# Optimization experiments

Measured on AMD Instinct MI355X. Metric: run time of the kernel, lower is better.

The kernel has to match this reference:

```python
import jax, jax.numpy as jnp
import numpy as np

B, S_IN, S_CTX = 2, 4096, 512
INPUT_DIM = CTX_DIM = DIM = 1024
NUM_HEADS = 16
HEAD_DIM = DIM // NUM_HEADS
BASE = 10000.0


def rms_norm(x, scale, eps=1e-6):
    xf = x.astype(jnp.float32)
    rrms = jax.lax.rsqrt(jnp.mean(xf * xf, axis=-1, keepdims=True) + eps)
    return (xf * rrms).astype(x.dtype) * scale


def apply_rope(x, pos):
    # x: [B, N, H, D]; rotate-half RoPE over full head_dim
    d = x.shape[-1]
    inv_freq = 1.0 / (BASE ** (jnp.arange(0, d, 2, dtype=jnp.float32) / d))  # [d/2]
    ang = pos.astype(jnp.float32)[:, None] * inv_freq[None, :]  # [N, d/2]
    cos = jnp.cos(ang)[None, :, None, :]
    sin = jnp.sin(ang)[None, :, None, :]
    x1, x2 = x[..., : d // 2], x[..., d // 2 :]
    return jnp.concatenate([x1 * cos - x2 * sin, x2 * cos + x1 * sin], axis=-1).astype(x.dtype)


def setup_inputs() -> dict:
    key = jax.random.key(0)
    ks = jax.random.split(key, 8)
    std = 0.02
    return {
        "input": jax.random.normal(ks[0], (B, S_IN, INPUT_DIM), jnp.float32),
        "context": jax.random.normal(ks[1], (B, S_CTX, CTX_DIM), jnp.float32),
        "W_qkv_in": jax.random.normal(ks[2], (3 * DIM, INPUT_DIM), jnp.float32) * std,
        "b_qkv_in": jnp.zeros((3 * DIM,), jnp.float32),
        "W_qkv_ctx": jax.random.normal(ks[3], (3 * DIM, CTX_DIM), jnp.float32) * std,
        "b_qkv_ctx": jnp.zeros((3 * DIM,), jnp.float32),
        "q_scale_in": jnp.ones((DIM,), jnp.float32),
        "k_scale_in": jnp.ones((DIM,), jnp.float32),
        "q_scale_ctx": jnp.ones((DIM,), jnp.float32),
        "k_scale_ctx": jnp.ones((DIM,), jnp.float32),
        "W_out_in": jax.random.normal(ks[4], (INPUT_DIM, DIM), jnp.float32) * std,
        "b_out_in": jnp.zeros((INPUT_DIM,), jnp.float32),
        "W_out_ctx": jax.random.normal(ks[5], (CTX_DIM, DIM), jnp.float32) * std,
        "b_out_ctx": jnp.zeros((CTX_DIM,), jnp.float32),
    }


def reference(input, context, W_qkv_in, b_qkv_in, W_qkv_ctx, b_qkv_ctx,
              q_scale_in, k_scale_in, q_scale_ctx, k_scale_ctx,
              W_out_in, b_out_in, W_out_ctx, b_out_ctx):
    # dual-stream QKV projections
    qkv_i = input @ W_qkv_in.T + b_qkv_in        # [B, S_in, 3*DIM]
    qkv_c = context @ W_qkv_ctx.T + b_qkv_ctx    # [B, S_ctx, 3*DIM]
    qi, ki, vi = jnp.split(qkv_i, 3, axis=-1)
    qc, kc, vc = jnp.split(qkv_c, 3, axis=-1)
    # QK-RMSNorm over full dim (as in QKNorm(dim))
    qi, ki = rms_norm(qi, q_scale_in), rms_norm(ki, k_scale_in)
    qc, kc = rms_norm(qc, q_scale_ctx), rms_norm(kc, k_scale_ctx)
    # concat context first, then input
    q = jnp.concatenate([qc, qi], axis=1)  # [B, N, DIM]
    k = jnp.concatenate([kc, ki], axis=1)
    v = jnp.concatenate([vc, vi], axis=1)
    N = q.shape[1]
    pos = jnp.arange(N)
    # RoPE applied per head
    q = apply_rope(q.reshape(B, N, NUM_HEADS, HEAD_DIM), pos).reshape(B, N, DIM)
    k = apply_rope(k.reshape(B, N, NUM_HEADS, HEAD_DIM), pos).reshape(B, N, DIM)
    # single-head attention over full dim (faithful to source: heads flattened before q@k^T)
    scale = HEAD_DIM ** -0.5
    attn = jax.nn.softmax(jnp.einsum('bnd,bmd->bnm', q, k) * scale, axis=-1)
    out = jnp.einsum('bnm,bmd->bnd', attn, v)  # [B, N, DIM]
    s_ctx = context.shape[1]
    input_output = out[:, s_ctx:, :] @ W_out_in.T + b_out_in
    context_output = out[:, :s_ctx, :] @ W_out_ctx.T + b_out_ctx
    return (input_output, context_output)
```

## Files before the change

### kernel.cpp

```cpp
#include <hip/hip_runtime.h>
#include <stdint.h>

typedef unsigned short u16;
typedef __bf16 bf16x8 __attribute__((ext_vector_type(8)));
typedef float f32x4 __attribute__((ext_vector_type(4)));

typedef const __attribute__((address_space(1))) uint32_t* gu32p;
typedef __attribute__((address_space(3))) uint32_t* lu32p;
#define GLOAD_LDS16(g, l) \
  __builtin_amdgcn_global_load_lds((gu32p)(const void*)(g), (lu32p)(void*)(l), 16, 0, 0)

static __device__ __forceinline__ u16 f2bf(float f) {
  uint32_t u = __builtin_bit_cast(uint32_t, f);
  return (u16)((u + 0x7FFFu + ((u >> 16) & 1u)) >> 16);
}
static __device__ __forceinline__ float bf2f(u16 h) {
  uint32_t u = ((uint32_t)h) << 16;
  return __builtin_bit_cast(float, u);
}

static __device__ __forceinline__ int xcd_swz(int bid, int nwg) {
  const int c = nwg >> 3;
  return (bid & 7) * c + (bid >> 3);
}

__global__ __launch_bounds__(256) void k_conv_all(
    const float* __restrict__ s0, u16* __restrict__ d0,
    const float* __restrict__ s1, u16* __restrict__ d1,
    const float* __restrict__ s2, u16* __restrict__ d2,
    const float* __restrict__ s3, u16* __restrict__ d3,
    const float* __restrict__ s4, u16* __restrict__ d4,
    const float* __restrict__ s5, u16* __restrict__ d5) {
  int b = blockIdx.x;
  const float* src; u16* dst; long off;
  if (b < 8192)       { src = s0; dst = d0; off = (long)b * 1024; }
  else if (b < 9216)  { src = s1; dst = d1; off = (long)(b - 8192) * 1024; }
  else if (b < 12288) { src = s2; dst = d2; off = (long)(b - 9216) * 1024; }
  else if (b < 15360) { src = s3; dst = d3; off = (long)(b - 12288) * 1024; }
  else if (b < 16384) { src = s4; dst = d4; off = (long)(b - 15360) * 1024; }
  else                { src = s5; dst = d5; off = (long)(b - 16384) * 1024; }
  long i = off + threadIdx.x * 4;
  const float4 v = *(const float4*)&src[i];
  ushort4 o;
  o.x = f2bf(v.x); o.y = f2bf(v.y); o.z = f2bf(v.z); o.w = f2bf(v.w);
  *(ushort4*)&dst[i] = o;
}

__device__ __forceinline__ void gemm_bk64(const u16* __restrict__ A, const u16* __restrict__ Bt,
                                          int lda, int ldb, long row0, long col0,
                                          int kbeg, int kend, u16* smem, f32x4 acc[4][4]) {
  const int tid = threadIdx.x;
  const int l = tid & 63;
  const int w = tid >> 6;
  const int wm = w >> 1, wn = w & 1;
  const int lr = l & 15, kg = l >> 4;
  const int swz = (lr & 7) * 8;
  const int r_l = tid >> 3;
  const int ssrc = ((tid & 7) ^ (r_l & 7)) * 8;
  const u16* gA = &A[(row0 + r_l) * (long)lda + ssrc];
  const u16* gB = &Bt[(col0 + r_l) * (long)ldb + ssrc];
  u16* const ldsA = smem + w * 512;
  u16* const ldsB = smem + 8192 + w * 512;
  const int NT = (kend - kbeg) >> 6;

  {
#pragma unroll
    for (int c = 0; c < 4; ++c) {
      GLOAD_LDS16(gA + (c * 32) * (long)lda + kbeg, ldsA + c * 2048);
      GLOAD_LDS16(gB + (c * 32) * (long)ldb + kbeg, ldsB + c * 2048);
    }
  }
  asm volatile("s_waitcnt vmcnt(0)" ::: "memory");
  __builtin_amdgcn_s_barrier();
  __builtin_amdgcn_sched_barrier(0);

  for (int t = 0; t < NT; ++t) {
    const int d = (t & 1) << 14;
    const int dn = ((t + 1) & 1) << 14;
    const bool pf = (t + 1 < NT);
    const long k1 = kbeg + (long)(t + 1) * 64;
    bf16x8 af[4], bv[4];
    if (pf) {
#pragma unroll
      for (int c = 0; c < 4; ++c)
        GLOAD_LDS16(gA + (c * 32) * (long)lda + k1, ldsA + dn + c * 2048);
    }
#pragma unroll
    for (int i = 0; i < 4; ++i) {
      af[i] = *(const bf16x8*)&smem[d + (wm * 64 + i * 16 + lr) * 64 + (kg * 8 ^ swz)];
      bv[i] = *(const bf16x8*)&smem[d + 8192 + (wn * 64 + i * 16 + lr) * 64 + (kg * 8 ^ swz)];
    }
    __builtin_amdgcn_s_setprio(1);
#pragma unroll
    for (int mf = 0; mf < 4; ++mf)
#pragma unroll
      for (int nf = 0; nf < 4; ++nf)
        acc[mf][nf] = __builtin_amdgcn_mfma_f32_16x16x32_bf16(af[mf], bv[nf], acc[mf][nf], 0, 0, 0);
    __builtin_amdgcn_s_setprio(0);
    if (pf) {
#pragma unroll
      for (int c = 0; c < 4; ++c)
        GLOAD_LDS16(gB + (c * 32) * (long)ldb + k1, ldsB + dn + c * 2048);
    }
#pragma unroll
    for (int i = 0; i < 4; ++i) {
      af[i] = *(const bf16x8*)&smem[d + (wm * 64 + i * 16 + lr) * 64 + ((32 + kg * 8) ^ swz)];
      bv[i] = *(const bf16x8*)&smem[d + 8192 + (wn * 64 + i * 16 + lr) * 64 + ((32 + kg * 8) ^ swz)];
    }
    __builtin_amdgcn_s_setprio(1);
#pragma unroll
    for (int mf = 0; mf < 4; ++mf)
#pragma unroll
      for (int nf = 0; nf < 4; ++nf)
        acc[mf][nf] = __builtin_amdgcn_mfma_f32_16x16x32_bf16(af[mf], bv[nf], acc[mf][nf], 0, 0, 0);
    __builtin_amdgcn_s_setprio(0);
    asm volatile("s_waitcnt vmcnt(0)" ::: "memory");
    __builtin_amdgcn_s_barrier();
    __builtin_amdgcn_sched_barrier(0);
  }
}

#define EPI_VARS                                   \
  const int l = threadIdx.x & 63;                  \
  const int w = threadIdx.x >> 6;                  \
  const int wm = w >> 1, wn = w & 1;               \
  const int mrow = (l >> 4) * 4, ncol = l & 15;

__global__ __launch_bounds__(256, 2) void k_gemm_qkv(
    const u16* __restrict__ XIN, const u16* __restrict__ XCTX,
    const u16* __restrict__ WQI, const u16* __restrict__ WQC,
    const float* __restrict__ bqi, const float* __restrict__ bqc,
    u16* __restrict__ qb, u16* __restrict__ kb, u16* __restrict__ vt) {
  __shared__ u16 smem[32768];
  f32x4 acc[4][4] = {};
  const int f = xcd_swz(blockIdx.x + 72 * blockIdx.y, 72 * 24);
  const int bx = f % 72, by = f / 72;
  const bool isCtx = bx >= 64;
  const u16* X = isCtx ? XCTX : XIN;
  const u16* W = isCtx ? WQC : WQI;
  const float* bias = isCtx ? bqc : bqi;
  const int seg_start = isCtx ? 0 : 512;
  long row0 = (long)(isCtx ? bx - 64 : bx) * 128;
  long col0 = (long)by * 128;
  gemm_bk64(X, W, 1024, 1024, row0, col0, 0, 1024, smem, acc);
  EPI_VARS
#pragma unroll
  for (int mf = 0; mf < 4; ++mf)
#pragma unroll
    for (int nf = 0; nf < 4; ++nf)
#pragma unroll
      for (int r = 0; r < 4; ++r) {
        int m = (int)row0 + wm * 64 + mf * 16 + mrow + r;
        int n = (int)col0 + wn * 64 + nf * 16 + ncol;
        float v = acc[mf][nf][r] + bias[n];
        int b, s;
        if (isCtx) { b = m >> 9; s = m & 511; } else { b = m >> 12; s = m & 4095; }
        long grow = (long)b * 4608 + seg_start + s;
        if (n < 1024)      qb[grow * 1024 + n] = f2bf(v);
        else if (n < 2048) kb[grow * 1024 + (n - 1024)] = f2bf(v);
        else               vt[((long)b * 1024 + (n - 2048)) * 4608 + seg_start + s] = f2bf(v);
      }
}

__global__ __launch_bounds__(256) void k_normrope(u16* __restrict__ qb, u16* __restrict__ kb,
                                                  const float* __restrict__ qsi, const float* __restrict__ ksi,
                                                  const float* __restrict__ qsc, const float* __restrict__ ksc) {
  __shared__ float sm[4];
  const int row = blockIdx.x;
  const int which = blockIdx.y;
  const int n = row % 4608;
  u16* buf = which ? kb : qb;
  const float* scale = which ? (n < 512 ? ksc : ksi) : (n < 512 ? qsc : qsi);
  u16* rp = buf + (long)row * 1024;
  const int t = threadIdx.x;
  const int h = t >> 4;
  const int jj = (t & 15) * 2;
  const int e1 = h * 64 + jj;
  const int e2 = e1 + 32;
  uint32_t u1 = *(const uint32_t*)&rp[e1];
  uint32_t u2 = *(const uint32_t*)&rp[e2];
  float x1a = bf2f((u16)u1), x1b = bf2f((u16)(u1 >> 16));
  float x2a = bf2f((u16)u2), x2b = bf2f((u16)(u2 >> 16));
  float ss = x1a * x1a + x1b * x1b + x2a * x2a + x2b * x2b;
#pragma unroll
  for (int o = 32; o; o >>= 1) ss += __shfl_xor(ss, o, 64);
  if ((t & 63) == 0) sm[t >> 6] = ss;
  __syncthreads();
  ss = sm[0] + sm[1] + sm[2] + sm[3];
  const float rr = rsqrtf(ss * (1.0f / 1024.0f) + 1e-6f);
  float s1a = scale[e1], s1b = scale[e1 + 1], s2a = scale[e2], s2b = scale[e2 + 1];
  x1a *= rr * s1a; x1b *= rr * s1b; x2a *= rr * s2a; x2b *= rr * s2b;
  const float c = -13.287712379549449f / 32.0f;
  float fa = exp2f((float)jj * c), fb = exp2f((float)(jj + 1) * c);
  float sna, csa, snb, csb;
  sincosf((float)n * fa, &sna, &csa);
  sincosf((float)n * fb, &snb, &csb);
  u16 o1a = f2bf(x1a * csa - x2a * sna), o1b = f2bf(x1b * csb - x2b * snb);
  u16 o2a = f2bf(x2a * csa + x1a * sna), o2b = f2bf(x2b * csb + x1b * snb);
  *(uint32_t*)&rp[e1] = (uint32_t)o1a | ((uint32_t)o1b << 16);
  *(uint32_t*)&rp[e2] = (uint32_t)o2a | ((uint32_t)o2b << 16);
}

__global__ __launch_bounds__(256, 2) void k_gemm_s(const u16* __restrict__ Q, const u16* __restrict__ Kb,
                                                   float* __restrict__ S) {
  __shared__ u16 smem[32768];
  f32x4 acc[4][4] = {};
  const int f = xcd_swz(blockIdx.x + 36 * blockIdx.y, 36 * 36);
  long row0 = (long)(f % 36) * 128;
  long col0 = (long)(f / 36) * 128;
  gemm_bk64(Q, Kb, 1024, 1024, row0, col0, 0, 1024, smem, acc);
  EPI_VARS
#pragma unroll
  for (int mf = 0; mf < 4; ++mf)
#pragma unroll
    for (int nf = 0; nf < 4; ++nf)
#pragma unroll
      for (int r = 0; r < 4; ++r) {
        long m = row0 + wm * 64 + mf * 16 + mrow + r;
        long n = col0 + wn * 64 + nf * 16 + ncol;
        S[m * 4608 + n] = acc[mf][nf][r] * 0.125f;
      }
}

__global__ __launch_bounds__(256) void k_softmax(const float* __restrict__ S, u16* __restrict__ P) {
  __shared__ float sm[4];
  const long row = blockIdx.x;
  const float* sr = S + row * 4608;
  const int t = threadIdx.x;
  float v[18];
  float mx = -3.4e38f;
#pragma unroll
  for (int i = 0; i < 18; ++i) { v[i] = sr[i * 256 + t]; mx = fmaxf(mx, v[i]); }
#pragma unroll
  for (int o = 32; o; o >>= 1) mx = fmaxf(mx, __shfl_xor(mx, o, 64));
  if ((t & 63) == 0) sm[t >> 6] = mx;
  __syncthreads();
  mx = fmaxf(fmaxf(sm[0], sm[1]), fmaxf(sm[2], sm[3]));
  __syncthreads();
  float sum = 0.f;
#pragma unroll
  for (int i = 0; i < 18; ++i) { v[i] = __expf(v[i] - mx); sum += v[i]; }
#pragma unroll
  for (int o = 32; o; o >>= 1) sum += __shfl_xor(sum, o, 64);
  if ((t & 63) == 0) sm[t >> 6] = sum;
  __syncthreads();
  sum = sm[0] + sm[1] + sm[2] + sm[3];
  const float inv = 1.0f / sum;
  u16* pr = P + row * 4608;
#pragma unroll
  for (int i = 0; i < 18; ++i) pr[i * 256 + t] = f2bf(v[i] * inv);
}

__global__ __launch_bounds__(256, 2) void k_gemm_o(const u16* __restrict__ P, const u16* __restrict__ VT,
                                                   float* __restrict__ OP) {
  __shared__ u16 smem[32768];
  f32x4 acc[4][4] = {};
  const int f = xcd_swz(blockIdx.x + 36 * blockIdx.y, 36 * 8);
  long row0 = (long)(f % 36) * 128;
  long col0 = (long)(f / 36) * 128;
  const int kc = blockIdx.z;
  gemm_bk64(P, VT, 4608, 4608, row0, col0, kc * 1152, (kc + 1) * 1152, smem, acc);
  float* op = OP + (long)kc * 4608 * 1024;
  EPI_VARS
#pragma unroll
  for (int mf = 0; mf < 4; ++mf)
#pragma unroll
    for (int nf = 0; nf < 4; ++nf)
#pragma unroll
      for (int r = 0; r < 4; ++r) {
        long m = row0 + wm * 64 + mf * 16 + mrow + r;
        long n = col0 + wn * 64 + nf * 16 + ncol;
        op[m * 1024 + n] = acc[mf][nf][r];
      }
}

__global__ __launch_bounds__(256) void k_reduce4(const float* __restrict__ OP, u16* __restrict__ AO) {
  const long st = 4608L * 1024;
  long i = ((long)blockIdx.x * 256 + threadIdx.x) * 4;
  float4 a = *(const float4*)&OP[i];
  float4 b = *(const float4*)&OP[i + st];
  float4 c = *(const float4*)&OP[i + 2 * st];
  float4 d = *(const float4*)&OP[i + 3 * st];
  ushort4 o;
  o.x = f2bf(a.x + b.x + c.x + d.x);
  o.y = f2bf(a.y + b.y + c.y + d.y);
  o.z = f2bf(a.z + b.z + c.z + d.z);
  o.w = f2bf(a.w + b.w + c.w + d.w);
  *(ushort4*)&AO[i] = o;
}

__global__ __launch_bounds__(256, 2) void k_gemm_out2(const u16* __restrict__ AO,
                                                      const u16* __restrict__ WOI, const u16* __restrict__ WOC,
                                                      const float* __restrict__ boi, const float* __restrict__ boc,
                                                      float* __restrict__ out) {
  __shared__ u16 smem[32768];
  f32x4 acc[4][4] = {};
  const int f = xcd_swz(blockIdx.x + 72 * blockIdx.y, 72 * 8);
  long row0 = (long)(f % 72) * 128;
  long col0 = (long)(f / 72) * 128;
  int b = (int)(row0 / 4608);
  int s0 = (int)(row0 % 4608);
  const bool ctx = s0 < 512;
  const u16* W = ctx ? WOC : WOI;
  const float* bias = ctx ? boc : boi;
  float* ob = ctx ? out + 8388608 + ((long)b * 512 + s0) * 1024
                  : out + ((long)b * 4096 + (s0 - 512)) * 1024;
  gemm_bk64(AO, W, 1024, 1024, row0, col0, 0, 1024, smem, acc);
  EPI_VARS
#pragma unroll
  for (int mf = 0; mf < 4; ++mf)
#pragma unroll
    for (int nf = 0; nf < 4; ++nf)
#pragma unroll
      for (int r = 0; r < 4; ++r) {
        long m = wm * 64 + mf * 16 + mrow + r;
        long n = col0 + wn * 64 + nf * 16 + ncol;
        ob[m * 1024 + n] = acc[mf][nf][r] + bias[n];
      }
}

extern "C" void kernel_launch(void* const* d_in, const int* in_sizes, int n_in,
                              void* d_out, int out_size, void* d_ws, size_t ws_size,
                              hipStream_t stream) {
  const float* input   = (const float*)d_in[0];
  const float* context = (const float*)d_in[1];
  const float* Wqi     = (const float*)d_in[2];
  const float* bqi     = (const float*)d_in[3];
  const float* Wqc     = (const float*)d_in[4];
  const float* bqc     = (const float*)d_in[5];
  const float* qsi     = (const float*)d_in[6];
  const float* ksi     = (const float*)d_in[7];
  const float* qsc     = (const float*)d_in[8];
  const float* ksc     = (const float*)d_in[9];
  const float* Woi     = (const float*)d_in[10];
  const float* boi     = (const float*)d_in[11];
  const float* Woc     = (const float*)d_in[12];
  const float* boc     = (const float*)d_in[13];
  float* out = (float*)d_out;

  uint8_t* ws = (uint8_t*)d_ws;
  u16* XIN  = (u16*)(ws + 0);
  u16* XCTX = (u16*)(ws + 16777216);
  u16* WQI  = (u16*)(ws + 18874368);
  u16* WQC  = (u16*)(ws + 25165824);
  u16* WOI  = (u16*)(ws + 31457280);
  u16* WOC  = (u16*)(ws + 33554432);
  u16* QB   = (u16*)(ws + 35651584);
  u16* KB   = (u16*)(ws + 54525952);
  u16* VT   = (u16*)(ws + 73400320);
  u16* AO   = (u16*)(ws + 92274688);
  float* S32 = (float*)(ws + 111149056);
  u16* PB   = (u16*)(ws + 196083712);

  k_conv_all<<<dim3(17408), 256, 0, stream>>>(input, XIN, context, XCTX, Wqi, WQI,
                                              Wqc, WQC, Woi, WOI, Woc, WOC);

  k_gemm_qkv<<<dim3(72, 24), 256, 0, stream>>>(XIN, XCTX, WQI, WQC, bqi, bqc, QB, KB, VT);

  k_normrope<<<dim3(9216, 2), 256, 0, stream>>>(QB, KB, qsi, ksi, qsc, ksc);

  for (int b = 0; b < 2; ++b) {
    const u16* Qb  = QB + (long)b * 4608 * 1024;
    const u16* Kbp = KB + (long)b * 4608 * 1024;
    const u16* VTb = VT + (long)b * 1024 * 4608;
    u16* AOb = AO + (long)b * 4608 * 1024;
    k_gemm_s<<<dim3(36, 36), 256, 0, stream>>>(Qb, Kbp, S32);
    k_softmax<<<dim3(4608), 256, 0, stream>>>(S32, PB);
    k_gemm_o<<<dim3(36, 8, 4), 256, 0, stream>>>(PB, VTb, (float*)S32);
    k_reduce4<<<dim3(4608), 256, 0, stream>>>((const float*)S32, AOb);
  }

  k_gemm_out2<<<dim3(72, 8), 256, 0, stream>>>(AO, WOI, WOC, boi, boc, out);
}
```

Before: 536.8 us.

## Switch GEMMs to 4-stage BK32 pipeline and drop XCD block swizzle

Replaces the double-buffered BK=64 GEMM mainloop with a four-buffer ring of BK=32 tiles that keeps three tiles in flight, using partial vmcnt waits and one barrier per iteration. The LDS swizzle is changed to suit 32-wide rows. The XCD-aware block-index remapping is also removed from all GEMM kernels, so they fall back to plain blockIdx tiling. The deeper prefetch is meant to hide global load latency better, but it halves the MFMA work per barrier and may lose L2 locality on the MI355X's multiple XCDs.

```diff
diff --git a/kernel.cpp b/kernel.cpp
--- a/kernel.cpp
+++ b/kernel.cpp
@@ -17,11 +17,6 @@
 static __device__ __forceinline__ float bf2f(u16 h) {
   uint32_t u = ((uint32_t)h) << 16;
   return __builtin_bit_cast(float, u);
-}
-
-static __device__ __forceinline__ int xcd_swz(int bid, int nwg) {
-  const int c = nwg >> 3;
-  return (bid & 7) * c + (bid >> 3);
 }
 
 __global__ __launch_bounds__(256) void k_conv_all(
@@ -46,49 +41,47 @@
   *(ushort4*)&dst[i] = o;
 }
 
-__device__ __forceinline__ void gemm_bk64(const u16* __restrict__ A, const u16* __restrict__ Bt,
-                                          int lda, int ldb, long row0, long col0,
-                                          int kbeg, int kend, u16* smem, f32x4 acc[4][4]) {
+__device__ __forceinline__ void gemm_p3(const u16* __restrict__ A, const u16* __restrict__ Bt,
+                                        int lda, int ldb, long row0, long col0,
+                                        int kbeg, int kend, u16* smem, f32x4 acc[4][4]) {
   const int tid = threadIdx.x;
   const int l = tid & 63;
   const int w = tid >> 6;
   const int wm = w >> 1, wn = w & 1;
   const int lr = l & 15, kg = l >> 4;
-  const int swz = (lr & 7) * 8;
-  const int r_l = tid >> 3;
-  const int ssrc = ((tid & 7) ^ (r_l & 7)) * 8;
+  const int rs = ((kg ^ ((lr >> 1) & 3)) * 8);
+  const int r_l = tid >> 2;
+  const int ssrc = ((tid & 3) ^ ((r_l >> 1) & 3)) * 8;
   const u16* gA = &A[(row0 + r_l) * (long)lda + ssrc];
   const u16* gB = &Bt[(col0 + r_l) * (long)ldb + ssrc];
-  u16* const ldsA = smem + w * 512;
-  u16* const ldsB = smem + 8192 + w * 512;
-  const int NT = (kend - kbeg) >> 6;
-
-  {
-#pragma unroll
-    for (int c = 0; c < 4; ++c) {
-      GLOAD_LDS16(gA + (c * 32) * (long)lda + kbeg, ldsA + c * 2048);
-      GLOAD_LDS16(gB + (c * 32) * (long)ldb + kbeg, ldsB + c * 2048);
-    }
+  const int wofs = w * 512;
+  const int NT = (kend - kbeg) >> 5;
+
+#define STAGE_TILE(tt, buf)                                         \
+  {                                                                 \
+    const long kk = kbeg + (long)(tt) * 32;                         \
+    u16* ba = smem + (buf) * 8192 + wofs;                           \
+    GLOAD_LDS16(gA + kk, ba);                                       \
+    GLOAD_LDS16(gA + 64 * (long)lda + kk, ba + 2048);               \
+    GLOAD_LDS16(gB + kk, ba + 4096);                                \
+    GLOAD_LDS16(gB + 64 * (long)ldb + kk, ba + 6144);               \
   }
-  asm volatile("s_waitcnt vmcnt(0)" ::: "memory");
+
+  STAGE_TILE(0, 0);
+  STAGE_TILE(1, 1);
+  STAGE_TILE(2, 2);
+  asm volatile("s_waitcnt vmcnt(8)" ::: "memory");
   __builtin_amdgcn_s_barrier();
   __builtin_amdgcn_sched_barrier(0);
 
   for (int t = 0; t < NT; ++t) {
-    const int d = (t & 1) << 14;
-    const int dn = ((t + 1) & 1) << 14;
-    const bool pf = (t + 1 < NT);
-    const long k1 = kbeg + (long)(t + 1) * 64;
+    if (t + 3 < NT) STAGE_TILE(t + 3, (t + 3) & 3);
+    const int d = (t & 3) * 8192;
     bf16x8 af[4], bv[4];
-    if (pf) {
-#pragma unroll
-      for (int c = 0; c < 4; ++c)
-        GLOAD_LDS16(gA + (c * 32) * (long)lda + k1, ldsA + dn + c * 2048);
-    }
 #pragma unroll
     for (int i = 0; i < 4; ++i) {
-      af[i] = *(const bf16x8*)&smem[d + (wm * 64 + i * 16 + lr) * 64 + (kg * 8 ^ swz)];
-      bv[i] = *(const bf16x8*)&smem[d + 8192 + (wn * 64 + i * 16 + lr) * 64 + (kg * 8 ^ swz)];
+      af[i] = *(const bf16x8*)&smem[d + (wm * 64 + i * 16 + lr) * 32 + rs];
+      bv[i] = *(const bf16x8*)&smem[d + 4096 + (wn * 64 + i * 16 + lr) * 32 + rs];
     }
     __builtin_amdgcn_s_setprio(1);
 #pragma unroll
@@ -97,27 +90,15 @@
       for (int nf = 0; nf < 4; ++nf)
         acc[mf][nf] = __builtin_amdgcn_mfma_f32_16x16x32_bf16(af[mf], bv[nf], acc[mf][nf], 0, 0, 0);
     __builtin_amdgcn_s_setprio(0);
-    if (pf) {
-#pragma unroll
-      for (int c = 0; c < 4; ++c)
-        GLOAD_LDS16(gB + (c * 32) * (long)ldb + k1, ldsB + dn + c * 2048);
+    if (t + 4 <= NT)      asm volatile("s_waitcnt vmcnt(8)" ::: "memory");
+    else if (t + 3 == NT) asm volatile("s_waitcnt vmcnt(4)" ::: "memory");
+    else if (t + 2 == NT) asm volatile("s_waitcnt vmcnt(0)" ::: "memory");
+    if (t + 1 < NT) {
+      __builtin_amdgcn_s_barrier();
+      __builtin_amdgcn_sched_barrier(0);
     }
-#pragma unroll
-    for (int i = 0; i < 4; ++i) {
-      af[i] = *(const bf16x8*)&smem[d + (wm * 64 + i * 16 + lr) * 64 + ((32 + kg * 8) ^ swz)];
-      bv[i] = *(const bf16x8*)&smem[d + 8192 + (wn * 64 + i * 16 + lr) * 64 + ((32 + kg * 8) ^ swz)];
-    }
-    __builtin_amdgcn_s_setprio(1);
-#pragma unroll
-    for (int mf = 0; mf < 4; ++mf)
-#pragma unroll
-      for (int nf = 0; nf < 4; ++nf)
-        acc[mf][nf] = __builtin_amdgcn_mfma_f32_16x16x32_bf16(af[mf], bv[nf], acc[mf][nf], 0, 0, 0);
-    __builtin_amdgcn_s_setprio(0);
-    asm volatile("s_waitcnt vmcnt(0)" ::: "memory");
-    __builtin_amdgcn_s_barrier();
-    __builtin_amdgcn_sched_barrier(0);
   }
+#undef STAGE_TILE
 }
 
 #define EPI_VARS                                   \
@@ -133,16 +114,14 @@
     u16* __restrict__ qb, u16* __restrict__ kb, u16* __restrict__ vt) {
   __shared__ u16 smem[32768];
   f32x4 acc[4][4] = {};
-  const int f = xcd_swz(blockIdx.x + 72 * blockIdx.y, 72 * 24);
-  const int bx = f % 72, by = f / 72;
-  const bool isCtx = bx >= 64;
+  const bool isCtx = blockIdx.x >= 64;
   const u16* X = isCtx ? XCTX : XIN;
   const u16* W = isCtx ? WQC : WQI;
   const float* bias = isCtx ? bqc : bqi;
   const int seg_start = isCtx ? 0 : 512;
-  long row0 = (long)(isCtx ? bx - 64 : bx) * 128;
-  long col0 = (long)by * 128;
-  gemm_bk64(X, W, 1024, 1024, row0, col0, 0, 1024, smem, acc);
+  long row0 = (long)(isCtx ? blockIdx.x - 64 : blockIdx.x) * 128;
+  long col0 = (long)blockIdx.y * 128;
+  gemm_p3(X, W, 1024, 1024, row0, col0, 0, 1024, smem, acc);
   EPI_VARS
 #pragma unroll
   for (int mf = 0; mf < 4; ++mf)
@@ -205,10 +184,9 @@
                                                    float* __restrict__ S) {
   __shared__ u16 smem[32768];
   f32x4 acc[4][4] = {};
-  const int f = xcd_swz(blockIdx.x + 36 * blockIdx.y, 36 * 36);
-  long row0 = (long)(f % 36) * 128;
-  long col0 = (long)(f / 36) * 128;
-  gemm_bk64(Q, Kb, 1024, 1024, row0, col0, 0, 1024, smem, acc);
+  long row0 = (long)blockIdx.x * 128;
+  long col0 = (long)blockIdx.y * 128;
+  gemm_p3(Q, Kb, 1024, 1024, row0, col0, 0, 1024, smem, acc);
   EPI_VARS
 #pragma unroll
   for (int mf = 0; mf < 4; ++mf)
@@ -255,11 +233,10 @@
                                                    float* __restrict__ OP) {
   __shared__ u16 smem[32768];
   f32x4 acc[4][4] = {};
-  const int f = xcd_swz(blockIdx.x + 36 * blockIdx.y, 36 * 8);
-  long row0 = (long)(f % 36) * 128;
-  long col0 = (long)(f / 36) * 128;
+  long row0 = (long)blockIdx.x * 128;
+  long col0 = (long)blockIdx.y * 128;
   const int kc = blockIdx.z;
-  gemm_bk64(P, VT, 4608, 4608, row0, col0, kc * 1152, (kc + 1) * 1152, smem, acc);
+  gemm_p3(P, VT, 4608, 4608, row0, col0, kc * 1152, (kc + 1) * 1152, smem, acc);
   float* op = OP + (long)kc * 4608 * 1024;
   EPI_VARS
 #pragma unroll
@@ -295,9 +272,8 @@
                                                       float* __restrict__ out) {
   __shared__ u16 smem[32768];
   f32x4 acc[4][4] = {};
-  const int f = xcd_swz(blockIdx.x + 72 * blockIdx.y, 72 * 8);
-  long row0 = (long)(f % 72) * 128;
-  long col0 = (long)(f / 72) * 128;
+  long row0 = (long)blockIdx.x * 128;
+  long col0 = (long)blockIdx.y * 128;
   int b = (int)(row0 / 4608);
   int s0 = (int)(row0 % 4608);
   const bool ctx = s0 < 512;
@@ -305,7 +281,7 @@
   const float* bias = ctx ? boc : boi;
   float* ob = ctx ? out + 8388608 + ((long)b * 512 + s0) * 1024
                   : out + ((long)b * 4096 + (s0 - 512)) * 1024;
-  gemm_bk64(AO, W, 1024, 1024, row0, col0, 0, 1024, smem, acc);
+  gemm_p3(AO, W, 1024, 1024, row0, col0, 0, 1024, smem, acc);
   EPI_VARS
 #pragma unroll
   for (int mf = 0; mf < 4; ++mf)
```

Measured after the change: 487.3 us. 9.2% less time.
